# Performance work log

Hardware: AMD Instinct MI355X
Metric: run time of the kernel (lower is better)

The kernel has to match this reference:

```python
import jax, jax.numpy as jnp
import numpy as np

B, S, H = 32, 512, 768
V = 8192
W_MAX = 256  # max words per sample after merging subwords


def setup_inputs() -> dict:
    key = jax.random.key(0)
    k1, k2, k3 = jax.random.split(key, 3)
    bert_encodings = jax.random.normal(k1, (B, S, H), dtype=jnp.float32)
    # per-token word index, sorted per row -> contiguous ragged segments
    segment_ids = jnp.sort(jax.random.randint(k2, (B, S), 0, W_MAX, dtype=jnp.int32), axis=1)
    W = jax.random.normal(k3, (H, V), dtype=jnp.float32) * 0.02
    b = jnp.zeros((V,), dtype=jnp.float32)
    return {
        "bert_encodings": bert_encodings,
        "segment_ids": segment_ids,
        "W": W,
        "b": b,
        "num_words": W_MAX,
    }


def reference(bert_encodings, segment_ids, W, b, num_words):
    Bb, Ss, Hh = bert_encodings.shape
    # Flatten batch: give each sample its own block of segment ids so one
    # segment_sum handles the whole batch (fused segment-reduce).
    flat_ids = (segment_ids + jnp.arange(Bb, dtype=segment_ids.dtype)[:, None] * num_words).reshape(-1)
    flat_enc = bert_encodings.reshape(-1, Hh)
    sums = jax.ops.segment_sum(flat_enc, flat_ids, num_segments=Bb * num_words)  # [B*W, H]
    counts = jax.ops.segment_sum(jnp.ones((Bb * Ss,), dtype=flat_enc.dtype), flat_ids,
                                 num_segments=Bb * num_words)  # [B*W]
    # mean per word; words with no subwords are zero-padded (like pad_sequence)
    denom = jnp.where(counts > 0, counts, 1.0)[:, None]
    merged = jnp.where(counts[:, None] > 0, sums / denom, 0.0).reshape(Bb, num_words, Hh)
    logits = jnp.einsum("bwh,hv->bwv", merged, W) + b  # [B, W_MAX, V]
    return logits
```

## Files before the change

kernel.cpp:

```cpp
#include <hip/hip_runtime.h>
#include <cstdint>
#include <cstddef>

typedef unsigned short ushort_t;
typedef __bf16 bf16x8 __attribute__((ext_vector_type(8)));
typedef float f32x4 __attribute__((ext_vector_type(4)));
typedef float f32x4v __attribute__((ext_vector_type(4)));
typedef unsigned short u16x4 __attribute__((ext_vector_type(4)));
typedef unsigned short u16x8 __attribute__((ext_vector_type(8)));

__device__ __forceinline__ ushort_t f2bf(float x) {
    union { float f; uint32_t u; } v; v.f = x;
    return (ushort_t)((v.u + 0x7FFFu + ((v.u >> 16) & 1u)) >> 16);
}

__device__ __forceinline__ void gld_lds16(const void* g, void* l) {
    __builtin_amdgcn_global_load_lds(
        (const __attribute__((address_space(1))) uint32_t*)g,
        (__attribute__((address_space(3))) uint32_t*)l,
        16, 0, 0);
}

__global__ __launch_bounds__(256) void transpose_convert(
    const float* __restrict__ Wm, ushort_t* __restrict__ Wt, int H, int V)
{
    __shared__ ushort_t tile[64][72];
    const int v0 = blockIdx.x * 64;
    const int k0 = blockIdx.y * 64;
    const int tid = threadIdx.x;

    #pragma unroll
    for (int p = 0; p < 4; ++p) {
        const int krow = p * 16 + (tid >> 4);
        const int vcol = (tid & 15) * 4;
        const f32x4v w = *(const f32x4v*)&Wm[(size_t)(k0 + krow) * V + v0 + vcol];
        tile[vcol + 0][krow] = f2bf(w.x);
        tile[vcol + 1][krow] = f2bf(w.y);
        tile[vcol + 2][krow] = f2bf(w.z);
        tile[vcol + 3][krow] = f2bf(w.w);
    }
    __syncthreads();
    #pragma unroll
    for (int p = 0; p < 2; ++p) {
        const int idx = p * 256 + tid;
        const int v = idx >> 3;
        const int c = (idx & 7) * 8;
        const u16x8 val = *(const u16x8*)&tile[v][c];
        *(u16x8*)&Wt[(size_t)(v0 + v) * H + k0 + c] = val;
    }
}

__global__ __launch_bounds__(256) void seg_mean(
    const float* __restrict__ enc,
    const int*   __restrict__ seg,
    ushort_t*    __restrict__ merged,
    int S, int H, int W)
{
    const int wave = threadIdx.x >> 6;
    const int lane = threadIdx.x & 63;
    const int bw = blockIdx.x * 4 + wave;
    const int b  = bw >> 8;
    const int w  = bw & 255;
    const int* srow = seg + (size_t)b * S;

    int l = 0, r = S;
    while (l < r) { int m = (l + r) >> 1; if (srow[m] < w) l = m + 1; else r = m; }
    const int lo = l;
    r = S;
    while (l < r) { int m = (l + r) >> 1; if (srow[m] < w + 1) l = m + 1; else r = m; }
    const int hi = l;

    const int cnt = hi - lo;
    const float scale = (cnt > 0) ? (1.0f / (float)cnt) : 0.0f;
    const float* erow = enc + (size_t)b * S * H;
    ushort_t* orow = merged + (size_t)bw * H;

    #pragma unroll
    for (int c = 0; c < 3; ++c) {
        const int col = c * 256 + lane * 4;
        f32x4v s = {0.f, 0.f, 0.f, 0.f};
        for (int t = lo; t < hi; ++t) {
            const f32x4v v = *(const f32x4v*)&erow[(size_t)t * H + col];
            s.x += v.x; s.y += v.y; s.z += v.z; s.w += v.w;
        }
        u16x4 o;
        o.x = f2bf(s.x * scale); o.y = f2bf(s.y * scale);
        o.z = f2bf(s.z * scale); o.w = f2bf(s.w * scale);
        *(u16x4*)&orow[col] = o;
    }
}


#define BAR() do { asm volatile("" ::: "memory"); \
                   __builtin_amdgcn_s_barrier(); \
                   asm volatile("" ::: "memory"); } while (0)

#define STG_A(U, S) do { \
    const ushort_t* g_ = Ag + (U) * 64 + (size_t)(S) * 64 * K; \
    char* l_ = ldsA + ((((U) & 1) * 2 + (S)) * 16384); \
    gld_lds16(g_, l_); \
    gld_lds16(g_ + (size_t)128 * K, l_ + 8192); \
} while (0)

#define STG_B(U, S) do { \
    const ushort_t* g_ = Bg + (U) * 64 + (size_t)(S) * 32 * K; \
    char* l_ = ldsB + ((((U) & 1) * 2 + (S)) * 16384); \
    gld_lds16(g_, l_); \
    gld_lds16(g_ + (size_t)128 * K, l_ + 8192); \
} while (0)

#define LDA(DST, MS, I, KK) \
    DST = *(const bf16x8*)(Ar + cur * 32768 + (MS) * 16384 + \
          (wm * 64 + (I) * 16 + r15) * 128 + (((KK) * 64 + quad * 16) ^ rswz))

#define LDB(DST, NS, J, KK) \
    DST = *(const bf16x8*)(Br + cur * 32768 + (NS) * 16384 + \
          (wn * 32 + (J) * 16 + r15) * 128 + (((KK) * 64 + quad * 16) ^ rswz))

#define MFMA_PH(MS, NS, BF) do { \
    __builtin_amdgcn_s_setprio(1); \
    _Pragma("unroll") \
    for (int i_ = 0; i_ < 4; ++i_) { \
      _Pragma("unroll") \
      for (int j_ = 0; j_ < 2; ++j_) { \
        acc[MS][i_][NS][j_] = __builtin_amdgcn_mfma_f32_16x16x32_bf16( \
            af[i_][0], BF[j_][0], acc[MS][i_][NS][j_], 0, 0, 0); \
        acc[MS][i_][NS][j_] = __builtin_amdgcn_mfma_f32_16x16x32_bf16( \
            af[i_][1], BF[j_][1], acc[MS][i_][NS][j_], 0, 0, 0); \
      } \
    } \
    __builtin_amdgcn_s_setprio(0); \
} while (0)

__global__ __launch_bounds__(512, 2) void gemm_bt256(
    const ushort_t* __restrict__ A,
    const ushort_t* __restrict__ Bt,
    const float*    __restrict__ bias,
    float*          __restrict__ C,
    int M, int N, int K)
{
    __shared__ ushort_t As[2][2][8192];
    __shared__ ushort_t Bs[2][2][8192];

    const int tid  = threadIdx.x;
    const int wave = tid >> 6;
    const int lane = tid & 63;
    const int r15  = lane & 15;
    const int quad = lane >> 4;
    const int wm   = wave >> 2;
    const int wn   = wave & 3;
    const int rswz = (r15 & 7) << 4;

    const int wg  = blockIdx.x;
    const int swz = (wg & 7) * 128 + (wg >> 3);
    const int m0  = (swz >> 5) * 256;
    const int n0  = (swz & 31) * 256;

    const int rho0 = tid >> 3;
    const int cBb  = (tid & 7) * 16;
    const int colA = (cBb ^ ((rho0 & 7) << 4)) >> 1;
    const int grB0 = ((rho0 >> 5) << 6) + (rho0 & 31);

    const ushort_t* Ag = A  + (size_t)(m0 + rho0) * K + colA;
    const ushort_t* Bg = Bt + (size_t)(n0 + grB0) * K + colA;
    char* ldsA = (char*)As + wave * 1024;
    char* ldsB = (char*)Bs + wave * 1024;
    const char* Ar = (const char*)As;
    const char* Br = (const char*)Bs;

    const int T = K >> 6;

    f32x4 acc[2][4][2][2] = {};

    STG_A(0, 0); STG_B(0, 0); STG_A(0, 1); STG_B(0, 1);
    STG_A(1, 0); STG_B(1, 0);
    asm volatile("s_waitcnt vmcnt(4)" ::: "memory");
    BAR();

    bf16x8 af[4][2], bf0[2][2], bf1[2][2];

    for (int t = 0; t < T; ++t) {
        const int cur = t & 1;
        int u1 = t + 1; if (u1 >= T) u1 = t - 1;
        int u2 = t + 2; if (u2 >= T) u2 = t;

        #pragma unroll
        for (int i = 0; i < 4; ++i) { LDA(af[i][0], 0, i, 0); LDA(af[i][1], 0, i, 1); }
        #pragma unroll
        for (int j = 0; j < 2; ++j) { LDB(bf0[j][0], 0, j, 0); LDB(bf0[j][1], 0, j, 1); }
        STG_A(u1, 1);
        BAR();
        MFMA_PH(0, 0, bf0);
        BAR();

        #pragma unroll
        for (int j = 0; j < 2; ++j) { LDB(bf1[j][0], 1, j, 0); LDB(bf1[j][1], 1, j, 1); }
        STG_B(u1, 1);
        BAR();
        MFMA_PH(0, 1, bf1);
        BAR();

        #pragma unroll
        for (int i = 0; i < 4; ++i) { LDA(af[i][0], 1, i, 0); LDA(af[i][1], 1, i, 1); }
        STG_A(u2, 0);
        BAR();
        MFMA_PH(1, 0, bf0);
        BAR();

        STG_B(u2, 0);
        BAR();
        MFMA_PH(1, 1, bf1);
        asm volatile("s_waitcnt vmcnt(4)" ::: "memory");
        BAR();
    }

    #pragma unroll
    for (int ms = 0; ms < 2; ++ms) {
        #pragma unroll
        for (int i = 0; i < 4; ++i) {
            const int row = m0 + wm * 128 + ms * 64 + i * 16 + quad * 4;
            #pragma unroll
            for (int ns = 0; ns < 2; ++ns) {
                #pragma unroll
                for (int j = 0; j < 2; ++j) {
                    const int col = n0 + wn * 64 + ns * 32 + j * 16 + r15;
                    const float bv = bias[col];
                    float* cp = C + (size_t)row * N + col;
                    #pragma unroll
                    for (int r = 0; r < 4; ++r)
                        cp[(size_t)r * N] = acc[ms][i][ns][j][r] + bv;
                }
            }
        }
    }
}

extern "C" void kernel_launch(void* const* d_in, const int* in_sizes, int n_in,
                              void* d_out, int out_size, void* d_ws, size_t ws_size,
                              hipStream_t stream) {
    const float* enc  = (const float*)d_in[0];
    const int*   seg  = (const int*)d_in[1];
    const float* Wm   = (const float*)d_in[2];
    const float* bias = (const float*)d_in[3];

    const int B = 32, S = 512, H = 768, V = 8192, WMAX = 256;
    const int M = B * WMAX;

    ushort_t* Wt     = (ushort_t*)d_ws;
    ushort_t* merged = Wt + (size_t)V * H;
    float*    out    = (float*)d_out;

    hipLaunchKernelGGL(transpose_convert, dim3(V / 64, H / 64), dim3(256), 0, stream,
                       Wm, Wt, H, V);
    hipLaunchKernelGGL(seg_mean, dim3(M / 4), dim3(256), 0, stream,
                       enc, seg, merged, S, H, WMAX);
    hipLaunchKernelGGL(gemm_bt256, dim3((M / 256) * (V / 256)), dim3(512), 0, stream,
                       merged, Wt, bias, out, M, V, H);
}
```

Measured before the change: 427.5 us.

## Fuse prep kernels, remap GEMM tiles per XCD, use nontemporal loads/stores

```diff
diff --git a/kernel.cpp b/kernel.cpp
--- a/kernel.cpp
+++ b/kernel.cpp
@@ -21,72 +21,77 @@
         16, 0, 0);
 }
 
-__global__ __launch_bounds__(256) void transpose_convert(
-    const float* __restrict__ Wm, ushort_t* __restrict__ Wt, int H, int V)
-{
-    __shared__ ushort_t tile[64][72];
-    const int v0 = blockIdx.x * 64;
-    const int k0 = blockIdx.y * 64;
-    const int tid = threadIdx.x;
-
-    #pragma unroll
-    for (int p = 0; p < 4; ++p) {
-        const int krow = p * 16 + (tid >> 4);
-        const int vcol = (tid & 15) * 4;
-        const f32x4v w = *(const f32x4v*)&Wm[(size_t)(k0 + krow) * V + v0 + vcol];
-        tile[vcol + 0][krow] = f2bf(w.x);
-        tile[vcol + 1][krow] = f2bf(w.y);
-        tile[vcol + 2][krow] = f2bf(w.z);
-        tile[vcol + 3][krow] = f2bf(w.w);
-    }
-    __syncthreads();
-    #pragma unroll
-    for (int p = 0; p < 2; ++p) {
-        const int idx = p * 256 + tid;
-        const int v = idx >> 3;
-        const int c = (idx & 7) * 8;
-        const u16x8 val = *(const u16x8*)&tile[v][c];
-        *(u16x8*)&Wt[(size_t)(v0 + v) * H + k0 + c] = val;
-    }
-}
-
-__global__ __launch_bounds__(256) void seg_mean(
+__global__ __launch_bounds__(256) void prep_fused(
+    const float* __restrict__ Wm,
+    ushort_t*    __restrict__ Wt,
     const float* __restrict__ enc,
     const int*   __restrict__ seg,
     ushort_t*    __restrict__ merged,
-    int S, int H, int W)
+    int H, int V, int S, int W)
 {
-    const int wave = threadIdx.x >> 6;
-    const int lane = threadIdx.x & 63;
-    const int bw = blockIdx.x * 4 + wave;
-    const int b  = bw >> 8;
-    const int w  = bw & 255;
-    const int* srow = seg + (size_t)b * S;
-
-    int l = 0, r = S;
-    while (l < r) { int m = (l + r) >> 1; if (srow[m] < w) l = m + 1; else r = m; }
-    const int lo = l;
-    r = S;
-    while (l < r) { int m = (l + r) >> 1; if (srow[m] < w + 1) l = m + 1; else r = m; }
-    const int hi = l;
-
-    const int cnt = hi - lo;
-    const float scale = (cnt > 0) ? (1.0f / (float)cnt) : 0.0f;
-    const float* erow = enc + (size_t)b * S * H;
-    ushort_t* orow = merged + (size_t)bw * H;
-
-    #pragma unroll
-    for (int c = 0; c < 3; ++c) {
-        const int col = c * 256 + lane * 4;
-        f32x4v s = {0.f, 0.f, 0.f, 0.f};
-        for (int t = lo; t < hi; ++t) {
-            const f32x4v v = *(const f32x4v*)&erow[(size_t)t * H + col];
-            s.x += v.x; s.y += v.y; s.z += v.z; s.w += v.w;
-        }
-        u16x4 o;
-        o.x = f2bf(s.x * scale); o.y = f2bf(s.y * scale);
-        o.z = f2bf(s.z * scale); o.w = f2bf(s.w * scale);
-        *(u16x4*)&orow[col] = o;
+    __shared__ ushort_t tile[64][72];
+    const int nT = (V / 64) * (H / 64);
+    const int tid = threadIdx.x;
+
+    if ((int)blockIdx.x < nT) {
+        const int v0 = (blockIdx.x % (V / 64)) * 64;
+        const int k0 = (blockIdx.x / (V / 64)) * 64;
+
+        #pragma unroll
+        for (int p = 0; p < 4; ++p) {
+            const int krow = p * 16 + (tid >> 4);
+            const int vcol = (tid & 15) * 4;
+            const f32x4v w = __builtin_nontemporal_load(
+                (const f32x4v*)&Wm[(size_t)(k0 + krow) * V + v0 + vcol]);
+            tile[vcol + 0][krow] = f2bf(w.x);
+            tile[vcol + 1][krow] = f2bf(w.y);
+            tile[vcol + 2][krow] = f2bf(w.z);
+            tile[vcol + 3][krow] = f2bf(w.w);
+        }
+        __syncthreads();
+        #pragma unroll
+        for (int p = 0; p < 2; ++p) {
+            const int idx = p * 256 + tid;
+            const int v = idx >> 3;
+            const int c = (idx & 7) * 8;
+            const u16x8 val = *(const u16x8*)&tile[v][c];
+            *(u16x8*)&Wt[(size_t)(v0 + v) * H + k0 + c] = val;
+        }
+    } else {
+        const int bx = (int)blockIdx.x - nT;
+        const int wave = tid >> 6;
+        const int lane = tid & 63;
+        const int bw = bx * 4 + wave;
+        const int b  = bw >> 8;
+        const int w  = bw & 255;
+        const int* srow = seg + (size_t)b * S;
+
+        int l = 0, r = S;
+        while (l < r) { int m = (l + r) >> 1; if (srow[m] < w) l = m + 1; else r = m; }
+        const int lo = l;
+        r = S;
+        while (l < r) { int m = (l + r) >> 1; if (srow[m] < w + 1) l = m + 1; else r = m; }
+        const int hi = l;
+
+        const int cnt = hi - lo;
+        const float scale = (cnt > 0) ? (1.0f / (float)cnt) : 0.0f;
+        const float* erow = enc + (size_t)b * S * H;
+        ushort_t* orow = merged + (size_t)bw * H;
+
+        #pragma unroll
+        for (int c = 0; c < 3; ++c) {
+            const int col = c * 256 + lane * 4;
+            f32x4v s = {0.f, 0.f, 0.f, 0.f};
+            for (int t = lo; t < hi; ++t) {
+                const f32x4v v = __builtin_nontemporal_load(
+                    (const f32x4v*)&erow[(size_t)t * H + col]);
+                s.x += v.x; s.y += v.y; s.z += v.z; s.w += v.w;
+            }
+            u16x4 o;
+            o.x = f2bf(s.x * scale); o.y = f2bf(s.y * scale);
+            o.z = f2bf(s.z * scale); o.w = f2bf(s.w * scale);
+            *(u16x4*)&orow[col] = o;
+        }
     }
 }
 
@@ -152,9 +157,14 @@
     const int rswz = (r15 & 7) << 4;
 
     const int wg  = blockIdx.x;
-    const int swz = (wg & 7) * 128 + (wg >> 3);
-    const int m0  = (swz >> 5) * 256;
-    const int n0  = (swz & 31) * 256;
+    const int xcd = wg & 7;
+    const int c_  = wg >> 3;
+    const int st  = xcd * 4 + (c_ >> 5);
+    const int idx = c_ & 31;
+    const int bm  = (st >> 2) * 4 + (idx >> 3);
+    const int bn  = (st & 3) * 8 + (idx & 7);
+    const int m0  = bm * 256;
+    const int n0  = bn * 256;
 
     const int rho0 = tid >> 3;
     const int cBb  = (tid & 7) * 16;
@@ -228,7 +238,8 @@
                     float* cp = C + (size_t)row * N + col;
                     #pragma unroll
                     for (int r = 0; r < 4; ++r)
-                        cp[(size_t)r * N] = acc[ms][i][ns][j][r] + bv;
+                        __builtin_nontemporal_store(acc[ms][i][ns][j][r] + bv,
+                                                    cp + (size_t)r * N);
                 }
             }
         }
@@ -250,10 +261,9 @@
     ushort_t* merged = Wt + (size_t)V * H;
     float*    out    = (float*)d_out;
 
-    hipLaunchKernelGGL(transpose_convert, dim3(V / 64, H / 64), dim3(256), 0, stream,
-                       Wm, Wt, H, V);
-    hipLaunchKernelGGL(seg_mean, dim3(M / 4), dim3(256), 0, stream,
-                       enc, seg, merged, S, H, WMAX);
+    const int nPrep = (V / 64) * (H / 64) + M / 4;
+    hipLaunchKernelGGL(prep_fused, dim3(nPrep), dim3(256), 0, stream,
+                       Wm, Wt, enc, seg, merged, H, V, S, WMAX);
     hipLaunchKernelGGL(gemm_bt256, dim3((M / 256) * (V / 256)), dim3(512), 0, stream,
                        merged, Wt, bias, out, M, V, H);
 }
```

Result: slower. 443.5 us (+3.7%).
